# Optimization experiments

Hardware: AMD Instinct MI355X
Metric: run time of the kernel (lower is better)

Reference implementation:

```python
import jax, jax.numpy as jnp
import numpy as np

INV_PI = 0.31830988618
PI_over_2 = 1.57079632679
PI_over_4 = 0.78539816339
N_MODES, DIM, COND_C = 8, 2, 64
LAYERS = [COND_C, 128, 512, 128, 32, N_MODES * DIM * 2 + N_MODES + 1]
N = 262144


def setup_inputs() -> dict:
    key = jax.random.key(0)
    ks = jax.random.split(key, 2 + 2 * (len(LAYERS) - 1))
    inp = {}
    inp["cond_vec"] = jax.random.normal(ks[0], (N, COND_C), jnp.float32)
    # uniforms in (0,1), bounded away from 0/1 so log/div are finite
    inp["randseed"] = jax.random.uniform(ks[1], (N, 2), jnp.float32, 1e-4, 1.0 - 1e-4)
    for i in range(len(LAYERS) - 1):
        inp[f"W{i}"] = jax.random.normal(ks[2 + 2 * i], (LAYERS[i], LAYERS[i + 1]), jnp.float32) * 0.01
        inp[f"b{i}"] = jnp.zeros((LAYERS[i + 1],), jnp.float32)
    return inp


def _mlp(x, Ws, bs):
    for i, (W, b) in enumerate(zip(Ws, bs)):
        x = x @ W + b
        if i < len(Ws) - 1:
            x = jax.nn.relu(x)
    return x


def _forward(cond_vec, randseed, Ws, bs):
    nm, d = N_MODES, DIM
    h = _mlp(cond_vec, Ws, bs)  # [N, nm*d*2 + nm + 1]
    loc = h[:, : nm * d].reshape(-1, nm, d)
    log_scale = h[:, nm * d : 2 * nm * d].reshape(-1, nm, d)
    w = jnp.abs(h[:, 2 * nm * d :])
    w = w / jnp.sum(w, axis=1, keepdims=True)  # [N, nm+1]
    wL = w[:, -1]

    r0, r1 = randseed[:, 0], randseed[:, 1]
    lambert_mask = r0 < wL
    gauss_mask = ~lambert_mask
    # in-place rescale of randseed column 0 in the torch code
    u0 = jnp.where(lambert_mask, r0 / wL, (r0 - wL) / (1.0 - wL))

    # --- gauss branch (Box-Muller) ---
    U1 = jnp.where(gauss_mask, u0, 0.5)  # masked positions: safe dummy
    U1 = jnp.maximum(U1, 1e-12)
    R = jnp.sqrt(-2.0 * jnp.log(U1))
    th = 2.0 * jnp.pi * r1
    eps_ = jnp.stack([R * jnp.cos(th), R * jnp.sin(th)], axis=-1)  # [N, 2]
    scale_sample = jnp.sum(jnp.exp(log_scale), axis=1)  # [N, 2]
    loc_sample = jnp.sum(loc, axis=1)  # [N, 2]
    z_gauss = eps_ * scale_sample + loc_sample

    # --- lambert branch (concentric disk map) ---
    wo0 = u0 * 2.0 - 1.0
    wo1 = r1 * 2.0 - 1.0
    nonzero = ~((wo0 == 0) & (wo1 == 0))
    cond1 = (jnp.abs(wo0) > jnp.abs(wo1)) & nonzero
    cond2 = (~cond1) & nonzero
    safe0 = jnp.where(wo0 == 0, 1.0, wo0)
    safe1 = jnp.where(wo1 == 0, 1.0, wo1)
    phi = jnp.where(cond1, PI_over_4 * wo1 / safe0, PI_over_2 - PI_over_4 * wo0 / safe1)
    r = jnp.where(cond1, wo0, jnp.where(cond2, wo1, 0.0))
    z_lambert = jnp.stack([r * jnp.cos(phi), r * jnp.sin(phi)], axis=-1)

    z = jnp.where(lambert_mask[:, None], z_lambert, z_gauss)  # [N, 2]

    # --- mixture log prob ---
    eps = (z[:, None, :] - loc) / jnp.exp(log_scale)  # [N, nm, 2]
    log_p = (-0.5 * d * jnp.log(2.0 * jnp.pi)
             + jnp.log(w[:, :-1] + 1e-5)
             - 0.5 * jnp.sum(eps ** 2, axis=2)
             - jnp.sum(log_scale, axis=2))  # [N, nm]
    pdf = jnp.where(z[:, 0] ** 2 + z[:, 1] ** 2 > 1.0, 0.0, INV_PI)
    lambert_log_p = jnp.log(pdf + 1e-5) + jnp.log(wL)
    log_p = jnp.concatenate([log_p, lambert_log_p[:, None]], axis=-1)  # [N, nm+1]
    return z, jax.scipy.special.logsumexp(log_p, axis=1)


def reference(cond_vec, randseed, W0, b0, W1, b1, W2, b2, W3, b3, W4, b4):
    Ws = [W0, W1, W2, W3, W4]
    bs = [b0, b1, b2, b3, b4]
    return _forward(cond_vec, randseed, Ws, bs)
```

## Files before the change

### kernel.cpp

```cpp
#include <hip/hip_runtime.h>
#include <math.h>

#define NTOT 262144
#define BROWS 64
#define THREADS 512
#define PITCH 140

typedef short bf16x8 __attribute__((ext_vector_type(8)));
typedef float f32x16 __attribute__((ext_vector_type(16)));

#define O0H 0
#define O0L 8192
#define O1H 16384
#define O1L 81920
#define O2H 147456
#define O2L 212992
#define GCNT_OFF 557056
#define GLIST_OFF 557120

#define SOFTBAR() asm volatile("s_waitcnt lgkmcnt(0)\n\ts_barrier" ::: "memory")

__device__ __forceinline__ unsigned short bf16_rne(float x){
    unsigned u = __float_as_uint(x);
    return (unsigned short)((u + 0x7FFFu + ((u >> 16) & 1u)) >> 16);
}
__device__ __forceinline__ void split2(float x, unsigned short& h, unsigned short& l){
    h = bf16_rne(x);
    float xh = __uint_as_float(((unsigned)h) << 16);
    l = bf16_rne(x - xh);
}

__device__ __forceinline__ int frag_off(int n, int k, int nks){
    return ((((n >> 5) * nks + (k >> 4)) << 9) | (((k >> 3) & 1) << 8) | ((n & 31) << 3) | (k & 7));
}

__global__ void prep_weights(const float* __restrict__ W0, const float* __restrict__ W1,
                             const float* __restrict__ W2, unsigned short* __restrict__ ws){
    int i = blockIdx.x * 256 + threadIdx.x;
    float v; int oh, ol;
    if (i < 8192){
        int n = i >> 6, k = i & 63; v = W0[k*128 + n];
        int o = frag_off(n, k, 4);  oh = O0H + o; ol = O0L + o;
    } else if (i < 73728){
        int j = i - 8192; int n = j >> 7, k = j & 127; v = W1[k*512 + n];
        int o = frag_off(n, k, 8);  oh = O1H + o; ol = O1L + o;
    } else if (i < 139264){
        int j = i - 73728; int n = j >> 9, k = j & 511; v = W2[k*128 + n];
        int o = frag_off(n, k, 32); oh = O2H + o; ol = O2L + o;
    } else return;
    unsigned short h, l; split2(v, h, l);
    ws[oh] = h; ws[ol] = l;
}

__device__ __forceinline__ void epilogue_row(const float* __restrict__ h, float r0v, float r1v,
        float& z0o, float& z1o, float& lseo, float& wLo, float& u0o, bool& lamo){
    float wraw[9]; float wsum = 0.0f;
    #pragma unroll
    for (int j = 0; j < 9; ++j){ wraw[j] = fabsf(h[32 + j]); wsum += wraw[j]; }
    float wL = wraw[8] / wsum;
    const bool lambert = r0v < wL;
    float u0 = lambert ? (r0v / wL) : ((r0v - wL) / (1.0f - wL));
    float U1 = lambert ? 0.5f : u0;
    U1 = fmaxf(U1, 1e-12f);
    float R  = sqrtf(-2.0f * logf(U1));
    float th = 6.28318530717958647692f * r1v;
    float ce = cosf(th), se = sinf(th);
    float es0[8], es1[8];
    float ssum0 = 0.0f, ssum1 = 0.0f, lsum0 = 0.0f, lsum1 = 0.0f;
    #pragma unroll
    for (int m = 0; m < 8; ++m){
        es0[m] = expf(h[16 + 2*m]); es1[m] = expf(h[16 + 2*m + 1]);
        ssum0 += es0[m]; ssum1 += es1[m];
        lsum0 += h[2*m]; lsum1 += h[2*m + 1];
    }
    float zg0 = (R * ce) * ssum0 + lsum0;
    float zg1 = (R * se) * ssum1 + lsum1;
    float wo0 = u0 * 2.0f - 1.0f;
    float wo1 = r1v * 2.0f - 1.0f;
    bool nonzero = !((wo0 == 0.0f) && (wo1 == 0.0f));
    bool c1 = (fabsf(wo0) > fabsf(wo1)) && nonzero;
    bool c2 = (!c1) && nonzero;
    float sa0 = (wo0 == 0.0f) ? 1.0f : wo0;
    float sa1 = (wo1 == 0.0f) ? 1.0f : wo1;
    float phi = c1 ? (0.78539816339f * wo1 / sa0)
                   : (1.57079632679f - 0.78539816339f * wo0 / sa1);
    float rr = c1 ? wo0 : (c2 ? wo1 : 0.0f);
    float zl0 = rr * cosf(phi);
    float zl1 = rr * sinf(phi);
    float z0 = lambert ? zl0 : zg0;
    float z1 = lambert ? zl1 : zg1;
    float lp[9];
    #pragma unroll
    for (int m = 0; m < 8; ++m){
        float e0 = (z0 - h[2*m])     / es0[m];
        float e1 = (z1 - h[2*m + 1]) / es1[m];
        float wm = wraw[m] / wsum;
        lp[m] = (-1.83787706640934548356f + logf(wm + 1e-5f))
                - 0.5f * (e0*e0 + e1*e1)
                - (h[16 + 2*m] + h[16 + 2*m + 1]);
    }
    float pdf = (z0*z0 + z1*z1 > 1.0f) ? 0.0f : 0.31830988618f;
    lp[8] = logf(pdf + 1e-5f) + logf(wL);
    float mx = lp[0];
    #pragma unroll
    for (int j = 1; j < 9; ++j) mx = fmaxf(mx, lp[j]);
    float s = 0.0f;
    #pragma unroll
    for (int j = 0; j < 9; ++j) s += expf(lp[j] - mx);
    z0o = z0; z1o = z1; lseo = mx + logf(s); wLo = wL; u0o = u0; lamo = lambert;
}

__device__ __forceinline__ bool flag_row(float r0v, float z0, float z1, float wL, float u0, bool lam){
    return (fabsf(r0v - wL) < 5e-3f)
        || (wL < 3e-3f) || (wL > 0.5f)
        || (fabsf(z0*z0 + z1*z1 - 1.0f) < (lam ? 0.02f : 0.2f))
        || (!lam && u0 < 3e-3f);
}

__device__ __forceinline__ f32x16 bias_init(const float* __restrict__ b, int mt, int lane, int nmax){
    f32x16 c;
    const int hq = ((lane >> 5) << 2);
    #pragma unroll
    for (int r = 0; r < 16; ++r){
        int n = mt + (r & 3) + ((r >> 2) << 3) + hq;
        c[r] = (n < nmax) ? b[n] : 0.0f;
    }
    return c;
}

__device__ __forceinline__ void write_tile(unsigned short* __restrict__ ah, unsigned short* __restrict__ al,
        int brow, int m0, int lane, const f32x16 acc, bool relu){
    const int hq = ((lane >> 5) << 2);
    #pragma unroll
    for (int q = 0; q < 4; ++q){
        ushort4 vh, vl;
        #pragma unroll
        for (int r = 0; r < 4; ++r){
            float x = acc[q*4 + r];
            if (relu) x = fmaxf(x, 0.0f);
            unsigned short hh, ll; split2(x, hh, ll);
            (&vh.x)[r] = hh; (&vl.x)[r] = ll;
        }
        const int off = brow*PITCH + m0 + q*8 + hq;
        *(ushort4*)(ah + off) = vh;
        *(ushort4*)(al + off) = vl;
    }
}

__device__ __forceinline__ void write_tile_f32t(float* __restrict__ dst,
        int brow, int m0, int lane, const f32x16 acc){
    const int hq = ((lane >> 5) << 2);
    #pragma unroll
    for (int q = 0; q < 4; ++q){
        #pragma unroll
        for (int r = 0; r < 4; ++r){
            int n = m0 + q*8 + hq + r;
            dst[n*64 + brow] = fmaxf(acc[q*4 + r], 0.0f);
        }
    }
}

__device__ __forceinline__ void load_half(const unsigned short* __restrict__ bh,
                                          const unsigned short* __restrict__ bl,
                                          int ks0, int lane, bf16x8* wh, bf16x8* wl){
    #pragma unroll
    for (int i = 0; i < 4; ++i){
        wh[i] = *(const bf16x8*)(bh + (ks0 + i)*512 + lane*8);
        wl[i] = *(const bf16x8*)(bl + (ks0 + i)*512 + lane*8);
    }
}

__device__ __forceinline__ void mfma_half(const bf16x8* wh, const bf16x8* wl,
        const unsigned short* __restrict__ acth, const unsigned short* __restrict__ actl,
        int ks0, int brow, int lane, f32x16& acc){
    const int kl = ((lane >> 5) << 3);
    #pragma unroll
    for (int i = 0; i < 4; ++i){
        const int k0 = (ks0 + i)*16 + kl;
        bf16x8 ah = *(const bf16x8*)(acth + brow*PITCH + k0);
        bf16x8 al = *(const bf16x8*)(actl + brow*PITCH + k0);
        acc = __builtin_amdgcn_mfma_f32_32x32x16_bf16(wh[i], ah, acc, 0, 0, 0);
        acc = __builtin_amdgcn_mfma_f32_32x32x16_bf16(wh[i], al, acc, 0, 0, 0);
        acc = __builtin_amdgcn_mfma_f32_32x32x16_bf16(wl[i], ah, acc, 0, 0, 0);
    }
}

__global__ __launch_bounds__(THREADS, 4)
void gmm_mfma(const float* __restrict__ cond, const float* __restrict__ rnd,
              const unsigned short* __restrict__ ws,
              const float* __restrict__ b0, const float* __restrict__ b1,
              const float* __restrict__ b2,
              const float* __restrict__ W3, const float* __restrict__ b3,
              const float* __restrict__ W4, const float* __restrict__ b4,
              int* __restrict__ gcnt, int* __restrict__ glist,
              float* __restrict__ out)
{
    extern __shared__ unsigned char smem[];
    unsigned short* aAh = (unsigned short*)smem;
    unsigned short* aAl = aAh + 64*PITCH;
    unsigned short* aBh = aAl + 64*PITCH;
    unsigned short* aBl = aBh + 64*PITCH;
    float* h2f = (float*)smem;
    float* h3f = (float*)(smem + 35840);
    float* h4f = (float*)(smem + 44032);

    const int tid  = threadIdx.x;
    const int lane = tid & 63;
    const int wv   = tid >> 6;
    const int row0 = blockIdx.x * BROWS;
    const int rg   = wv & 1;
    const int ct   = wv >> 1;
    const int brow = rg*32 + (lane & 31);
    const int m0   = ct * 32;
    const int kl   = ((lane >> 5) << 3);

    bf16x8 whA[4], wlA[4], whB[4], wlB[4];

    {
        f32x16 acc0 = bias_init(b0, m0, lane, 128);
        #pragma unroll 2
        for (int ks = 0; ks < 4; ++ks){
            const int k0 = ks*16 + kl;
            const float* cp = cond + (size_t)(row0 + brow)*64 + k0;
            float4 ca = *(const float4*)cp;
            float4 cb = *(const float4*)(cp + 4);
            float xs[8] = {ca.x, ca.y, ca.z, ca.w, cb.x, cb.y, cb.z, cb.w};
            bf16x8 ah, al;
            #pragma unroll
            for (int j = 0; j < 8; ++j){
                unsigned short hh, ll; split2(xs[j], hh, ll);
                ah[j] = (short)hh; al[j] = (short)ll;
            }
            bf16x8 wh = *(const bf16x8*)(ws + O0H + (ct*4 + ks)*512 + lane*8);
            bf16x8 wl = *(const bf16x8*)(ws + O0L + (ct*4 + ks)*512 + lane*8);
            acc0 = __builtin_amdgcn_mfma_f32_32x32x16_bf16(wh, ah, acc0, 0, 0, 0);
            acc0 = __builtin_amdgcn_mfma_f32_32x32x16_bf16(wh, al, acc0, 0, 0, 0);
            acc0 = __builtin_amdgcn_mfma_f32_32x32x16_bf16(wl, ah, acc0, 0, 0, 0);
        }
        write_tile(aAh, aAl, brow, m0, lane, acc0, true);
    }
    load_half(ws + O1H + (size_t)(ct*8)*512, ws + O1L + (size_t)(ct*8)*512, 0, lane, whA, wlA);
    SOFTBAR();

    f32x16 acc2 = bias_init(b2, m0, lane, 128);
    for (int c = 0; c < 4; ++c){
        const unsigned short* b1h = ws + O1H + (size_t)((c*4 + ct)*8)*512;
        const unsigned short* b1l = ws + O1L + (size_t)((c*4 + ct)*8)*512;
        const unsigned short* b2h = ws + O2H + (size_t)(ct*32 + c*8)*512;
        const unsigned short* b2l = ws + O2L + (size_t)(ct*32 + c*8)*512;
        f32x16 a1 = bias_init(b1 + c*128, m0, lane, 128);
        load_half(b1h, b1l, 4, lane, whB, wlB);
        mfma_half(whA, wlA, aAh, aAl, 0, brow, lane, a1);
        load_half(b2h, b2l, 0, lane, whA, wlA);
        mfma_half(whB, wlB, aAh, aAl, 4, brow, lane, a1);
        load_half(b2h, b2l, 4, lane, whB, wlB);
        SOFTBAR();
        write_tile(aBh, aBl, brow, m0, lane, a1, true);
        SOFTBAR();
        mfma_half(whA, wlA, aBh, aBl, 0, brow, lane, acc2);
        if (c < 3)
            load_half(ws + O1H + (size_t)(((c+1)*4 + ct)*8)*512,
                      ws + O1L + (size_t)(((c+1)*4 + ct)*8)*512, 0, lane, whA, wlA);
        mfma_half(whB, wlB, aBh, aBl, 4, brow, lane, acc2);
    }
    write_tile_f32t(h2f, brow, m0, lane, acc2);
    SOFTBAR();

    {
        const int row = tid & 63;
        const int nb  = tid >> 6;
        float acc[4];
        #pragma unroll
        for (int c = 0; c < 4; ++c) acc[c] = b3[nb*4 + c];
        #pragma unroll 8
        for (int k = 0; k < 128; ++k){
            float a = h2f[k*64 + row];
            const float* wr = W3 + k*32 + nb*4;
            #pragma unroll
            for (int c = 0; c < 4; ++c) acc[c] = fmaf(a, wr[c], acc[c]);
        }
        SOFTBAR();
        #pragma unroll
        for (int c = 0; c < 4; ++c) h3f[(nb*4 + c)*64 + row] = fmaxf(acc[c], 0.0f);
    }
    SOFTBAR();

    {
        const int row = tid & 63;
        const int nb  = tid >> 6;
        float acc[6];
        #pragma unroll
        for (int c = 0; c < 6; ++c){ int n = nb*6 + c; acc[c] = (n < 41) ? b4[n] : 0.0f; }
        #pragma unroll 8
        for (int k = 0; k < 32; ++k){
            float a = h3f[k*64 + row];
            const float* wr = W4 + k*41;
            #pragma unroll
            for (int c = 0; c < 6; ++c){ int n = nb*6 + c; if (n < 41) acc[c] = fmaf(a, wr[n], acc[c]); }
        }
        #pragma unroll
        for (int c = 0; c < 6; ++c){ int n = nb*6 + c; if (n < 41) h4f[n*64 + row] = acc[c]; }
    }
    SOFTBAR();

    if (tid < 64){
        const int row  = tid;
        const int grow = row0 + row;
        float h[41];
        #pragma unroll
        for (int j = 0; j < 41; ++j) h[j] = h4f[j*64 + row];
        float2 rv = *(const float2*)(rnd + 2*(size_t)grow);
        float z0, z1, lse, wL, u0; bool lam;
        epilogue_row(h, rv.x, rv.y, z0, z1, lse, wL, u0, lam);
        ((float2*)out)[grow] = make_float2(z0, z1);
        out[(size_t)2*NTOT + grow] = lse;
        if (flag_row(rv.x, z0, z1, wL, u0, lam)){
            int idx = atomicAdd(gcnt, 1); glist[idx] = grow;
        }
    }
}

__global__ __launch_bounds__(512, 2)
void gmm_fix(const float* __restrict__ cond, const float* __restrict__ rnd,
             const float* __restrict__ W0, const float* __restrict__ b0,
             const float* __restrict__ W1, const float* __restrict__ b1,
             const float* __restrict__ W2, const float* __restrict__ b2,
             const float* __restrict__ W3, const float* __restrict__ b3,
             const float* __restrict__ W4, const float* __restrict__ b4,
             const int* __restrict__ gcnt, const int* __restrict__ glist,
             float* __restrict__ out)
{
    __shared__ float fb[7296];
    float* c0g = fb;
    float* f0g = fb + 512;
    float* f1g = fb + 1536;
    float* f2g = fb + 5632;
    float* f3g = fb + 6656;
    float* h4g = fb + 6912;
    const int tid = threadIdx.x;
    const int nflag = *gcnt;

    for (int base = blockIdx.x * 8; base < nflag; base += gridDim.x * 8){
        const int g = min(8, nflag - base);
        {
            int i = tid >> 6, k = tid & 63;
            if (i < g) c0g[i*64 + k] = cond[(size_t)glist[base + i]*64 + k];
        }
        __syncthreads();
        if (tid < 128){
            float acc[8];
            #pragma unroll
            for (int i = 0; i < 8; ++i) acc[i] = b0[tid];
            #pragma unroll 8
            for (int k = 0; k < 64; ++k){
                float w = W0[k*128 + tid];
                #pragma unroll
                for (int i = 0; i < 8; ++i) acc[i] = fmaf(c0g[i*64 + k], w, acc[i]);
            }
            for (int i = 0; i < g; ++i) f0g[i*128 + tid] = fmaxf(acc[i], 0.0f);
        }
        __syncthreads();
        {
            float acc[8];
            #pragma unroll
            for (int i = 0; i < 8; ++i) acc[i] = b1[tid];
            #pragma unroll 8
            for (int k = 0; k < 128; ++k){
                float w = W1[k*512 + tid];
                #pragma unroll
                for (int i = 0; i < 8; ++i) acc[i] = fmaf(f0g[i*128 + k], w, acc[i]);
            }
            for (int i = 0; i < g; ++i) f1g[i*512 + tid] = fmaxf(acc[i], 0.0f);
        }
        __syncthreads();
        if (tid < 128){
            float acc[8];
            #pragma unroll
            for (int i = 0; i < 8; ++i) acc[i] = b2[tid];
            #pragma unroll 8
            for (int k = 0; k < 512; ++k){
                float w = W2[k*128 + tid];
                #pragma unroll
                for (int i = 0; i < 8; ++i) acc[i] = fmaf(f1g[i*512 + k], w, acc[i]);
            }
            for (int i = 0; i < g; ++i) f2g[i*128 + tid] = fmaxf(acc[i], 0.0f);
        }
        __syncthreads();
        if (tid < 32){
            float acc[8];
            #pragma unroll
            for (int i = 0; i < 8; ++i) acc[i] = b3[tid];
            #pragma unroll 8
            for (int k = 0; k < 128; ++k){
                float w = W3[k*32 + tid];
                #pragma unroll
                for (int i = 0; i < 8; ++i) acc[i] = fmaf(f2g[i*128 + k], w, acc[i]);
            }
            for (int i = 0; i < g; ++i) f3g[i*32 + tid] = fmaxf(acc[i], 0.0f);
        }
        __syncthreads();
        if (tid < 41){
            float acc[8];
            #pragma unroll
            for (int i = 0; i < 8; ++i) acc[i] = b4[tid];
            #pragma unroll 8
            for (int k = 0; k < 32; ++k){
                float w = W4[k*41 + tid];
                #pragma unroll
                for (int i = 0; i < 8; ++i) acc[i] = fmaf(f3g[i*32 + k], w, acc[i]);
            }
            for (int i = 0; i < g; ++i) h4g[i*48 + tid] = acc[i];
        }
        __syncthreads();
        if (tid < g){
            const int grow = glist[base + tid];
            float2 rv = *(const float2*)(rnd + 2*(size_t)grow);
            float z0, z1, lse, wL, u0; bool lam;
            epilogue_row(&h4g[tid*48], rv.x, rv.y, z0, z1, lse, wL, u0, lam);
            ((float2*)out)[grow] = make_float2(z0, z1);
            out[(size_t)2*NTOT + grow] = lse;
        }
        __syncthreads();
    }
}

extern "C" void kernel_launch(void* const* d_in, const int* in_sizes, int n_in,
                              void* d_out, int out_size, void* d_ws, size_t ws_size,
                              hipStream_t stream) {
    const float* cond = (const float*)d_in[0];
    const float* rnd  = (const float*)d_in[1];
    const float* W0 = (const float*)d_in[2];  const float* b0 = (const float*)d_in[3];
    const float* W1 = (const float*)d_in[4];  const float* b1 = (const float*)d_in[5];
    const float* W2 = (const float*)d_in[6];  const float* b2 = (const float*)d_in[7];
    const float* W3 = (const float*)d_in[8];  const float* b3 = (const float*)d_in[9];
    const float* W4 = (const float*)d_in[10]; const float* b4 = (const float*)d_in[11];
    float* out = (float*)d_out;
    unsigned short* ws = (unsigned short*)d_ws;
    int* gcnt  = (int*)((char*)d_ws + GCNT_OFF);
    int* glist = (int*)((char*)d_ws + GLIST_OFF);

    hipMemsetAsync(gcnt, 0, 4, stream);
    hipLaunchKernelGGL(prep_weights, dim3(544), dim3(256), 0, stream, W0, W1, W2, ws);

    hipLaunchKernelGGL(gmm_mfma, dim3(NTOT / BROWS), dim3(THREADS), 71680, stream,
                       cond, rnd, ws, b0, b1, b2, W3, b3, W4, b4, gcnt, glist, out);

    hipLaunchKernelGGL(gmm_fix, dim3(1024), dim3(512), 0, stream,
                       cond, rnd, W0, b0, W1, b1, W2, b2, W3, b3, W4, b4, gcnt, glist, out);
}
```

Measured before the change: 864.2 us.

## Pipeline weight loads with inline-asm global loads and explicit vmcnt waits

Replaces the compiler-generated weight fragment loads in the layer-1/layer-2 loop with inline-asm global_load_dwordx4 that use scalar base pointers. Explicit s_waitcnt vmcnt counts and sched barriers let the next half's loads stay in flight while the current MFMAs run, and the loop is fully unrolled. The b1 and b2 biases are staged in LDS, which adds about 2.5KB of shared memory per block. That could reduce occupancy, and the hand-placed waitcnt ordering is fragile.

Result: faster. 841.9 us (-2.6%).

```diff
diff --git a/kernel.cpp b/kernel.cpp
--- a/kernel.cpp
+++ b/kernel.cpp
@@ -19,6 +19,16 @@
 #define GLIST_OFF 557120
 
 #define SOFTBAR() asm volatile("s_waitcnt lgkmcnt(0)\n\ts_barrier" ::: "memory")
+
+#define WAITV(N) do{ asm volatile("s_waitcnt vmcnt(" #N ")" ::: "memory"); \
+                     __builtin_amdgcn_sched_barrier(0); }while(0)
+
+#define LOADG4(r0, r1, r2, r3, base) do{ \
+    asm volatile("global_load_dwordx4 %0, %1, %2 offset:0"    : "=v"(r0) : "v"(voff), "s"(base)); \
+    asm volatile("global_load_dwordx4 %0, %1, %2 offset:1024" : "=v"(r1) : "v"(voff), "s"(base)); \
+    asm volatile("global_load_dwordx4 %0, %1, %2 offset:2048" : "=v"(r2) : "v"(voff), "s"(base)); \
+    asm volatile("global_load_dwordx4 %0, %1, %2 offset:3072" : "=v"(r3) : "v"(voff), "s"(base)); \
+}while(0)
 
 __device__ __forceinline__ unsigned short bf16_rne(float x){
     unsigned u = __float_as_uint(x);
@@ -157,16 +167,6 @@
             int n = m0 + q*8 + hq + r;
             dst[n*64 + brow] = fmaxf(acc[q*4 + r], 0.0f);
         }
-    }
-}
-
-__device__ __forceinline__ void load_half(const unsigned short* __restrict__ bh,
-                                          const unsigned short* __restrict__ bl,
-                                          int ks0, int lane, bf16x8* wh, bf16x8* wl){
-    #pragma unroll
-    for (int i = 0; i < 4; ++i){
-        wh[i] = *(const bf16x8*)(bh + (ks0 + i)*512 + lane*8);
-        wl[i] = *(const bf16x8*)(bl + (ks0 + i)*512 + lane*8);
     }
 }
 
@@ -203,6 +203,8 @@
     float* h2f = (float*)smem;
     float* h3f = (float*)(smem + 35840);
     float* h4f = (float*)(smem + 44032);
+    float* b1g = (float*)(smem + 71680);
+    float* b2g = b1g + 512;
 
     const int tid  = threadIdx.x;
     const int lane = tid & 63;
@@ -213,8 +215,12 @@
     const int brow = rg*32 + (lane & 31);
     const int m0   = ct * 32;
     const int kl   = ((lane >> 5) << 3);
+    const unsigned voff = (unsigned)lane * 16;
 
     bf16x8 whA[4], wlA[4], whB[4], wlB[4];
+
+    b1g[tid >= 512 ? 0 : tid] = b1[tid >= 512 ? 0 : tid];
+    if (tid < 128) b2g[tid] = b2[tid];
 
     {
         f32x16 acc0 = bias_init(b0, m0, lane, 128);
@@ -239,28 +245,53 @@
         }
         write_tile(aAh, aAl, brow, m0, lane, acc0, true);
     }
-    load_half(ws + O1H + (size_t)(ct*8)*512, ws + O1L + (size_t)(ct*8)*512, 0, lane, whA, wlA);
+
+    asm volatile("s_waitcnt vmcnt(0)" ::: "memory");
+    __builtin_amdgcn_sched_barrier(0);
+    {
+        const unsigned short* p1h = ws + O1H + __builtin_amdgcn_readfirstlane(ct*4096);
+        const unsigned short* p1l = ws + O1L + __builtin_amdgcn_readfirstlane(ct*4096);
+        LOADG4(whA[0], whA[1], whA[2], whA[3], p1h);
+        LOADG4(wlA[0], wlA[1], wlA[2], wlA[3], p1l);
+    }
     SOFTBAR();
 
-    f32x16 acc2 = bias_init(b2, m0, lane, 128);
+    f32x16 acc2 = bias_init(b2g, m0, lane, 128);
+    #pragma unroll
     for (int c = 0; c < 4; ++c){
-        const unsigned short* b1h = ws + O1H + (size_t)((c*4 + ct)*8)*512;
-        const unsigned short* b1l = ws + O1L + (size_t)((c*4 + ct)*8)*512;
-        const unsigned short* b2h = ws + O2H + (size_t)(ct*32 + c*8)*512;
-        const unsigned short* b2l = ws + O2L + (size_t)(ct*32 + c*8)*512;
-        f32x16 a1 = bias_init(b1 + c*128, m0, lane, 128);
-        load_half(b1h, b1l, 4, lane, whB, wlB);
+        const unsigned short* b1h = ws + O1H + __builtin_amdgcn_readfirstlane((c*4 + ct)*4096);
+        const unsigned short* b1l = ws + O1L + __builtin_amdgcn_readfirstlane((c*4 + ct)*4096);
+        const unsigned short* c2h = ws + O2H + __builtin_amdgcn_readfirstlane((ct*32 + c*8)*512);
+        const unsigned short* c2l = ws + O2L + __builtin_amdgcn_readfirstlane((ct*32 + c*8)*512);
+
+        LOADG4(whB[0], whB[1], whB[2], whB[3], b1h + 2048);
+        LOADG4(wlB[0], wlB[1], wlB[2], wlB[3], b1l + 2048);
+        WAITV(8);
+        f32x16 a1 = bias_init(b1g + c*128, m0, lane, 128);
         mfma_half(whA, wlA, aAh, aAl, 0, brow, lane, a1);
-        load_half(b2h, b2l, 0, lane, whA, wlA);
+
+        LOADG4(whA[0], whA[1], whA[2], whA[3], c2h);
+        LOADG4(wlA[0], wlA[1], wlA[2], wlA[3], c2l);
+        WAITV(8);
         mfma_half(whB, wlB, aAh, aAl, 4, brow, lane, a1);
-        load_half(b2h, b2l, 4, lane, whB, wlB);
+
+        LOADG4(whB[0], whB[1], whB[2], whB[3], c2h + 2048);
+        LOADG4(wlB[0], wlB[1], wlB[2], wlB[3], c2l + 2048);
         SOFTBAR();
         write_tile(aBh, aBl, brow, m0, lane, a1, true);
         SOFTBAR();
+        WAITV(8);
         mfma_half(whA, wlA, aBh, aBl, 0, brow, lane, acc2);
-        if (c < 3)
-            load_half(ws + O1H + (size_t)(((c+1)*4 + ct)*8)*512,
-                      ws + O1L + (size_t)(((c+1)*4 + ct)*8)*512, 0, lane, whA, wlA);
+
+        if (c < 3){
+            const unsigned short* n1h = ws + O1H + __builtin_amdgcn_readfirstlane(((c+1)*4 + ct)*4096);
+            const unsigned short* n1l = ws + O1L + __builtin_amdgcn_readfirstlane(((c+1)*4 + ct)*4096);
+            LOADG4(whA[0], whA[1], whA[2], whA[3], n1h);
+            LOADG4(wlA[0], wlA[1], wlA[2], wlA[3], n1l);
+            WAITV(8);
+        } else {
+            WAITV(0);
+        }
         mfma_half(whB, wlB, aBh, aBl, 4, brow, lane, acc2);
     }
     write_tile_f32t(h2f, brow, m0, lane, acc2);
@@ -442,7 +473,7 @@
     hipMemsetAsync(gcnt, 0, 4, stream);
     hipLaunchKernelGGL(prep_weights, dim3(544), dim3(256), 0, stream, W0, W1, W2, ws);
 
-    hipLaunchKernelGGL(gmm_mfma, dim3(NTOT / BROWS), dim3(THREADS), 71680, stream,
+    hipLaunchKernelGGL(gmm_mfma, dim3(NTOT / BROWS), dim3(THREADS), 74240, stream,
                        cond, rnd, ws, b0, b1, b2, W3, b3, W4, b4, gcnt, glist, out);
 
     hipLaunchKernelGGL(gmm_fix, dim3(1024), dim3(512), 0, stream,
```
